# Performance work log

Hardware: AMD Instinct MI355X
Metric: run time of the kernel (lower is better)

Reference implementation:

```python
import jax, jax.numpy as jnp
import numpy as np

N_NODES = 100000
N_EDGES = 1600000
D_IN = 128
D_OUT = 128
SLOPE = 0.2


def setup_inputs() -> dict:
    key = jax.random.key(0)
    k1, k2, k3, k4 = jax.random.split(key, 4)
    x = jax.random.normal(k1, (N_NODES, D_IN), dtype=jnp.float32)
    edge_index = jax.random.randint(k2, (2, N_EDGES), 0, N_NODES, dtype=jnp.int64)
    scale = 1.0 / np.sqrt(D_IN)
    W_l = jax.random.normal(k3, (D_OUT, D_IN), dtype=jnp.float32) * scale
    b_l = jnp.zeros((D_OUT,), dtype=jnp.float32)
    W_r = jax.random.normal(k4, (D_OUT, D_IN), dtype=jnp.float32) * scale
    return {"x": x, "edge_index": edge_index, "W_l": W_l, "b_l": b_l, "W_r": W_r}


def reference(x, edge_index, W_l, b_l, W_r):
    # SAGEConv with mean aggregation: out = lin_l(mean_{j in N(i)} x_j) + lin_r(x_i)
    src = edge_index[0]  # message sources (x_j)
    dst = edge_index[1]  # aggregation targets (node i)
    n = x.shape[0]
    msg = x[src]  # [E, D_IN] gather
    summed = jax.ops.segment_sum(msg, dst, num_segments=n)  # [N, D_IN]
    cnt = jax.ops.segment_sum(jnp.ones((src.shape[0],), x.dtype), dst, num_segments=n)
    agg = summed / jnp.maximum(cnt, 1.0)[:, None]  # mean; zero-degree -> 0
    out = agg @ W_l.T + b_l + x @ W_r.T  # lin_l has bias, lin_r bias=False (PyG)
    # LeakyReLU(slope); Dropout(0.5) is identity in eval mode
    return jnp.where(out > 0, out, SLOPE * out)
```

## Files before the change

kernel.cpp:

```cpp
#include <hip/hip_runtime.h>

#define D 128
#define N_SCAN 1024
#define BSH 7
#define MAXBINS 1024

typedef float  f32x4  __attribute__((ext_vector_type(4)));
typedef short  s16x8  __attribute__((ext_vector_type(8)));
typedef unsigned short us8 __attribute__((ext_vector_type(8)));

__device__ __forceinline__ unsigned short f2bf(float f) {
    unsigned b = __float_as_uint(f);
    return (unsigned short)((b + 0x7fffu + ((b >> 16) & 1u)) >> 16);
}
__device__ __forceinline__ float bf2f(unsigned short u) {
    return __uint_as_float((unsigned)u << 16);
}

__global__ __launch_bounds__(256) void bin_hist(
    const int* __restrict__ dst, int* __restrict__ bincnt, int E, int BINS)
{
    __shared__ int h[MAXBINS];
    for (int b = threadIdx.x; b < BINS; b += 256) h[b] = 0;
    __syncthreads();
    int base = blockIdx.x * 4096;
    #pragma unroll
    for (int j = 0; j < 16; ++j) {
        int e = base + j * 256 + threadIdx.x;
        if (e < E) atomicAdd(&h[dst[e] >> BSH], 1);
    }
    __syncthreads();
    for (int b = threadIdx.x; b < BINS; b += 256)
        if (h[b]) atomicAdd(&bincnt[b], h[b]);
}

__global__ __launch_bounds__(256) void bin_scan(
    const int* __restrict__ bincnt, int* __restrict__ binptr,
    int* __restrict__ binhead, int* __restrict__ rowptr,
    int BINS, int N, int E)
{
    __shared__ int sl[256];
    const int t = threadIdx.x;
    int v[4];
    int s = 0;
    #pragma unroll
    for (int j = 0; j < 4; ++j) {
        int i = t * 4 + j;
        int c = (i < BINS) ? bincnt[i] : 0;
        v[j] = s;
        s += c;
    }
    sl[t] = s;
    __syncthreads();
    for (int off = 1; off < 256; off <<= 1) {
        int add = (t >= off) ? sl[t - off] : 0;
        __syncthreads();
        sl[t] += add;
        __syncthreads();
    }
    int excl = sl[t] - s;
    #pragma unroll
    for (int j = 0; j < 4; ++j) {
        int i = t * 4 + j;
        if (i < BINS) { binptr[i] = excl + v[j]; binhead[i] = excl + v[j]; }
    }
    if (t == 0) { binptr[BINS] = E; rowptr[N] = E; }
}

__global__ __launch_bounds__(256) void partition_edges(
    const int* __restrict__ src, const int* __restrict__ dst,
    int* __restrict__ binhead, unsigned* __restrict__ packed_g, int E, int BINS)
{
    __shared__ int h[MAXBINS];
    __shared__ int goff[MAXBINS];
    __shared__ int fill[MAXBINS];
    const int t = threadIdx.x;
    for (int b = t; b < BINS; b += 256) { h[b] = 0; fill[b] = 0; }
    __syncthreads();
    int base = blockIdx.x * 4096;
    int eb[16];
    unsigned pk[16];
    #pragma unroll
    for (int j = 0; j < 16; ++j) {
        int e = base + j * 256 + t;
        if (e < E) {
            int d = dst[e], s = src[e];
            eb[j] = d >> BSH;
            pk[j] = ((unsigned)(d & ((1 << BSH) - 1)) << 17) | (unsigned)s;
            atomicAdd(&h[eb[j]], 1);
        } else eb[j] = -1;
    }
    __syncthreads();
    for (int b = t; b < BINS; b += 256)
        if (h[b]) goff[b] = atomicAdd(&binhead[b], h[b]);
    __syncthreads();
    #pragma unroll
    for (int j = 0; j < 16; ++j) {
        if (eb[j] >= 0) {
            int p = goff[eb[j]] + atomicAdd(&fill[eb[j]], 1);
            packed_g[p] = pk[j];
        }
    }
}

__global__ __launch_bounds__(256) void bin_finalize(
    const unsigned* __restrict__ packed_g, const int* __restrict__ binptr,
    int* __restrict__ rowptr, int* __restrict__ srcs, int N)
{
    const int bin = blockIdx.x, t = threadIdx.x;
    const int beg = binptr[bin], end = binptr[bin + 1];
    const int node0 = bin << BSH;
    __shared__ int c[128];
    __shared__ int pf[128];
    __shared__ int hd[128];
    if (t < 128) c[t] = 0;
    __syncthreads();
    for (int i = beg + t; i < end; i += 256)
        atomicAdd(&c[packed_g[i] >> 17], 1);
    __syncthreads();
    if (t < 128) pf[t] = c[t];
    __syncthreads();
    for (int off = 1; off < 128; off <<= 1) {
        int v = 0;
        if (t < 128 && t >= off) v = pf[t - off];
        __syncthreads();
        if (t < 128) pf[t] += v;
        __syncthreads();
    }
    if (t < 128) {
        int node = node0 + t;
        if (node < N) {
            int r = beg + pf[t] - c[t];
            rowptr[node] = r;
            hd[t] = r;
        }
    }
    __syncthreads();
    for (int i = beg + t; i < end; i += 256) {
        unsigned p = packed_g[i];
        int dl = p >> 17;
        int s = p & 0x1FFFF;
        int pos = atomicAdd(&hd[dl], 1);
        srcs[pos] = s << 8;
    }
}

__global__ __launch_bounds__(256) void hist_kernel(
    const int* __restrict__ dst, int* __restrict__ cnt, int E)
{
    int e = blockIdx.x * 256 + threadIdx.x;
    if (e < E) atomicAdd(&cnt[dst[e]], 1);
}

__global__ __launch_bounds__(256) void scan1_kernel(
    const int* __restrict__ cnt, int* __restrict__ rowptr,
    int* __restrict__ blocksum, int N)
{
    __shared__ int sl[256];
    const int t = threadIdx.x;
    const int base = blockIdx.x * N_SCAN + t * 4;
    int v[4];
    int s = 0;
    #pragma unroll
    for (int j = 0; j < 4; ++j) {
        int i = base + j;
        int c = (i < N) ? cnt[i] : 0;
        v[j] = s;
        s += c;
    }
    sl[t] = s;
    __syncthreads();
    for (int off = 1; off < 256; off <<= 1) {
        int add = (t >= off) ? sl[t - off] : 0;
        __syncthreads();
        sl[t] += add;
        __syncthreads();
    }
    int incl = sl[t];
    int excl = incl - s;
    #pragma unroll
    for (int j = 0; j < 4; ++j) {
        int i = base + j;
        if (i < N) rowptr[i] = excl + v[j];
    }
    if (t == 255) blocksum[blockIdx.x] = incl;
}

__global__ void scan2_kernel(const int* __restrict__ blocksum,
                             int* __restrict__ blockoff, int nblk)
{
    if (threadIdx.x == 0 && blockIdx.x == 0) {
        int s = 0;
        for (int b = 0; b < nblk; ++b) { blockoff[b] = s; s += blocksum[b]; }
    }
}

__global__ __launch_bounds__(256) void scan3_kernel(
    int* __restrict__ rowptr, const int* __restrict__ blockoff,
    int* __restrict__ head, int N, int E)
{
    int i = blockIdx.x * 256 + threadIdx.x;
    if (i < N) {
        int r = rowptr[i] + blockoff[i >> 10];
        rowptr[i] = r;
        head[i] = r;
    } else if (i == N) {
        rowptr[N] = E;
    }
}

__global__ __launch_bounds__(256) void scatter_edges(
    const int* __restrict__ src, const int* __restrict__ dst,
    int* __restrict__ head, int* __restrict__ srcs, int E)
{
    int e = blockIdx.x * 256 + threadIdx.x;
    if (e < E) {
        int pos = atomicAdd(&head[dst[e]], 1);
        srcs[pos] = src[e];
    }
}

__global__ __launch_bounds__(256) void convert_bf16(
    const float* __restrict__ x, unsigned short* __restrict__ xb, long long total)
{
    long long i = ((long long)blockIdx.x * 256 + threadIdx.x) * 8;
    if (i >= total) return;
    float4 f0 = *(const float4*)(x + i);
    float4 f1 = *(const float4*)(x + i + 4);
    us8 u;
    u[0] = f2bf(f0.x); u[1] = f2bf(f0.y); u[2] = f2bf(f0.z); u[3] = f2bf(f0.w);
    u[4] = f2bf(f1.x); u[5] = f2bf(f1.y); u[6] = f2bf(f1.z); u[7] = f2bf(f1.w);
    *(us8*)(xb + i) = u;
}

__global__ __launch_bounds__(256) void aggregate_row(
    const unsigned short* __restrict__ xb, const int* __restrict__ rowptr,
    const int* __restrict__ srcs, unsigned short* __restrict__ aggb, int N)
{
    int wid  = (blockIdx.x * 256 + threadIdx.x) >> 6;
    int lane = threadIdx.x & 63;
    if (wid >= N) return;
    const int beg = rowptr[wid], end = rowptr[wid + 1];
    const char* xbase = (const char*)xb;

    float accL = 0.f, accH = 0.f;
    for (int b = beg; b < end; b += 64) {
        int idx = b + lane;
        int srcv = srcs[idx < end ? idx : end - 1];
        int cnt = end - b; if (cnt > 64) cnt = 64;
        int i = 0;
        for (; i + 8 <= cnt; i += 8) {
            unsigned u[8];
            #pragma unroll
            for (int j = 0; j < 8; ++j) {
                int so = __builtin_amdgcn_readlane(srcv, i + j);
                u[j] = *(const unsigned*)(xbase + so + lane * 4);
            }
            #pragma unroll
            for (int j = 0; j < 8; ++j) {
                accL += __uint_as_float(u[j] << 16);
                accH += __uint_as_float(u[j] & 0xffff0000u);
            }
        }
        for (; i < cnt; ++i) {
            int so = __builtin_amdgcn_readlane(srcv, i);
            unsigned u = *(const unsigned*)(xbase + so + lane * 4);
            accL += __uint_as_float(u << 16);
            accH += __uint_as_float(u & 0xffff0000u);
        }
    }
    float inv = 1.0f / fmaxf((float)(end - beg), 1.0f);
    unsigned lo = f2bf(accL * inv);
    unsigned hi = f2bf(accH * inv);
    ((unsigned*)aggb)[(size_t)wid * 64 + lane] = lo | (hi << 16);
}

__global__ __launch_bounds__(256) void aggregate_bf16(
    const unsigned short* __restrict__ xb, const int* __restrict__ rowptr,
    const int* __restrict__ srcs, unsigned short* __restrict__ aggb, int N)
{
    int wid  = (blockIdx.x * 256 + threadIdx.x) >> 6;
    int lane = threadIdx.x & 63;
    if (wid >= N) return;
    int beg = rowptr[wid], end = rowptr[wid + 1];
    const int q  = lane >> 4;
    const int sl = lane & 15;

    float acc[8] = {};
    int e = beg;
    for (; e + 8 <= end; e += 8) {
        int s0 = srcs[e + q];
        int s1 = srcs[e + 4 + q];
        us8 v0 = *(const us8*)(xb + (long long)s0 * D + sl * 8);
        us8 v1 = *(const us8*)(xb + (long long)s1 * D + sl * 8);
        #pragma unroll
        for (int j = 0; j < 8; ++j) acc[j] += bf2f(v0[j]);
        #pragma unroll
        for (int j = 0; j < 8; ++j) acc[j] += bf2f(v1[j]);
    }
    for (; e < end; e += 4) {
        int ee = e + q;
        if (ee < end) {
            int s0 = srcs[ee];
            us8 v0 = *(const us8*)(xb + (long long)s0 * D + sl * 8);
            #pragma unroll
            for (int j = 0; j < 8; ++j) acc[j] += bf2f(v0[j]);
        }
    }
    #pragma unroll
    for (int j = 0; j < 8; ++j) {
        acc[j] += __shfl_xor(acc[j], 16, 64);
        acc[j] += __shfl_xor(acc[j], 32, 64);
    }
    float inv = 1.0f / fmaxf((float)(end - beg), 1.0f);
    if (q == 0) {
        us8 u;
        #pragma unroll
        for (int j = 0; j < 8; ++j) u[j] = f2bf(acc[j] * inv);
        *(us8*)(aggb + (long long)wid * D + sl * 8) = u;
    }
}

__global__ __launch_bounds__(256) void convert_w_frag(
    const float* __restrict__ Wl, const float* __restrict__ Wr,
    unsigned short* __restrict__ wbf)
{
    int c = blockIdx.x * 256 + threadIdx.x;
    if (c >= 4096) return;
    int l  = c & 63;
    int ts = c >> 6;
    int t  = ts >> 3, s = ts & 7;
    int o  = t * 16 + (l & 15);
    int k2 = s * 32 + (l >> 4) * 8;
    const float* srcw = (k2 < 128) ? (Wl + o * D + k2) : (Wr + o * D + (k2 - 128));
    float4 f0 = *(const float4*)(srcw);
    float4 f1 = *(const float4*)(srcw + 4);
    us8 u;
    u[0] = f2bf(f0.x); u[1] = f2bf(f0.y); u[2] = f2bf(f0.z); u[3] = f2bf(f0.w);
    u[4] = f2bf(f1.x); u[5] = f2bf(f1.y); u[6] = f2bf(f1.z); u[7] = f2bf(f1.w);
    ((us8*)wbf)[c] = u;
}

__global__ __launch_bounds__(256) void mm_mfma3(
    const unsigned short* __restrict__ xb,
    const unsigned short* __restrict__ aggb,
    const unsigned short* __restrict__ wfrag,
    const float* __restrict__ bl,
    float* __restrict__ out, int N)
{
    const int tid  = threadIdx.x;
    const int lane = tid & 63;
    const int wv   = tid >> 6;
    const long long m0 = (long long)blockIdx.x * 128 + wv * 32;
    const int arow = lane & 15;
    const int kq   = lane >> 4;
    const long long r0 = m0 + arow;
    const long long r1 = m0 + 16 + arow;
    const bool v0 = (r0 < N), v1 = (r1 < N);
    const unsigned short* a0 = aggb + r0 * D + kq * 8;
    const unsigned short* x0 = xb   + r0 * D + kq * 8;
    const unsigned short* a1 = aggb + r1 * D + kq * 8;
    const unsigned short* x1 = xb   + r1 * D + kq * 8;
    const s16x8* wf = (const s16x8*)wfrag;

    f32x4 acc0[8] = {};
    f32x4 acc1[8] = {};

    #pragma unroll
    for (int s = 0; s < 8; ++s) {
        s16x8 af0 = {0, 0, 0, 0, 0, 0, 0, 0};
        s16x8 af1 = {0, 0, 0, 0, 0, 0, 0, 0};
        if (v0) af0 = *(const s16x8*)((s < 4) ? (a0 + s * 32) : (x0 + (s - 4) * 32));
        if (v1) af1 = *(const s16x8*)((s < 4) ? (a1 + s * 32) : (x1 + (s - 4) * 32));
        #pragma unroll
        for (int t = 0; t < 8; ++t) {
            s16x8 bf = wf[(t * 8 + s) * 64 + lane];
            acc0[t] = __builtin_amdgcn_mfma_f32_16x16x32_bf16(af0, bf, acc0[t], 0, 0, 0);
            acc1[t] = __builtin_amdgcn_mfma_f32_16x16x32_bf16(af1, bf, acc1[t], 0, 0, 0);
        }
    }

    const int crow = (lane >> 4) * 4;
    const int ccol = lane & 15;
    #pragma unroll
    for (int t = 0; t < 8; ++t) {
        int col = t * 16 + ccol;
        float bb = bl[col];
        #pragma unroll
        for (int r = 0; r < 4; ++r) {
            long long row0 = m0 + crow + r;
            if (row0 < N) {
                float vv = acc0[t][r] + bb;
                out[row0 * D + col] = vv > 0.f ? vv : 0.2f * vv;
            }
            long long row1 = m0 + 16 + crow + r;
            if (row1 < N) {
                float vv = acc1[t][r] + bb;
                out[row1 * D + col] = vv > 0.f ? vv : 0.2f * vv;
            }
        }
    }
}

__global__ __launch_bounds__(256) void mm_mfma(
    const unsigned short* __restrict__ xb,
    const unsigned short* __restrict__ aggb,
    const float* __restrict__ Wl, const float* __restrict__ bl,
    const float* __restrict__ Wr,
    float* __restrict__ out, int N)
{
    __shared__ char wlds[64 * 1024];
    const int tid = threadIdx.x;

    for (int c = tid; c < 4096; c += 256) {
        int byte = c * 16;
        int o  = byte >> 9;
        int k2 = (byte & 511) >> 1;
        const float* srcw = (k2 < 128) ? (Wl + o * D + k2) : (Wr + o * D + (k2 - 128));
        float4 f0 = *(const float4*)(srcw);
        float4 f1 = *(const float4*)(srcw + 4);
        us8 u;
        u[0] = f2bf(f0.x); u[1] = f2bf(f0.y); u[2] = f2bf(f0.z); u[3] = f2bf(f0.w);
        u[4] = f2bf(f1.x); u[5] = f2bf(f1.y); u[6] = f2bf(f1.z); u[7] = f2bf(f1.w);
        *(us8*)(wlds + (byte ^ ((o & 7) << 4))) = u;
    }
    __syncthreads();

    const int lane = tid & 63;
    const int wv   = tid >> 6;
    const long long m0 = (long long)blockIdx.x * 64 + wv * 16;
    const int arow = lane & 15;
    const int kq   = lane >> 4;
    const long long mrow = m0 + arow;
    const bool valid = (mrow < N);
    const unsigned short* aP = aggb + mrow * D + kq * 8;
    const unsigned short* xP = xb   + mrow * D + kq * 8;

    f32x4 acc[8] = {};

    #pragma unroll
    for (int s = 0; s < 8; ++s) {
        s16x8 afrag = {0, 0, 0, 0, 0, 0, 0, 0};
        if (valid) {
            const unsigned short* ap = (s < 4) ? (aP + s * 32) : (xP + (s - 4) * 32);
            afrag = *(const s16x8*)ap;
        }
        #pragma unroll
        for (int t = 0; t < 8; ++t) {
            int o = t * 16 + arow;
            int boff = (o << 9) + s * 64 + kq * 16;
            boff ^= (o & 7) << 4;
            s16x8 bfrag = *(const s16x8*)(wlds + boff);
            acc[t] = __builtin_amdgcn_mfma_f32_16x16x32_bf16(afrag, bfrag, acc[t], 0, 0, 0);
        }
    }

    const int crow = (lane >> 4) * 4;
    const int ccol = lane & 15;
    #pragma unroll
    for (int t = 0; t < 8; ++t) {
        int col = t * 16 + ccol;
        float bb = bl[col];
        #pragma unroll
        for (int r = 0; r < 4; ++r) {
            long long row = m0 + crow + r;
            if (row < N) {
                float v = acc[t][r] + bb;
                out[row * D + col] = v > 0.f ? v : 0.2f * v;
            }
        }
    }
}

__global__ __launch_bounds__(256) void aggregate_f32(
    const float* __restrict__ x, const int* __restrict__ rowptr,
    const int* __restrict__ srcs, float* __restrict__ out, int N)
{
    int wid  = (blockIdx.x * 256 + threadIdx.x) >> 6;
    int lane = threadIdx.x & 63;
    if (wid >= N) return;
    int beg = rowptr[wid], end = rowptr[wid + 1];
    const float2* x2 = (const float2*)x;
    float ax = 0.f, ay = 0.f;
    int e = beg;
    for (; e + 4 <= end; e += 4) {
        int s0 = srcs[e], s1 = srcs[e + 1], s2 = srcs[e + 2], s3 = srcs[e + 3];
        float2 v0 = x2[(long long)s0 * 64 + lane];
        float2 v1 = x2[(long long)s1 * 64 + lane];
        float2 v2 = x2[(long long)s2 * 64 + lane];
        float2 v3 = x2[(long long)s3 * 64 + lane];
        ax += v0.x + v1.x + v2.x + v3.x;
        ay += v0.y + v1.y + v2.y + v3.y;
    }
    for (; e < end; ++e) {
        float2 v = x2[(long long)srcs[e] * 64 + lane];
        ax += v.x; ay += v.y;
    }
    float inv = 1.0f / fmaxf((float)(end - beg), 1.0f);
    float2 o; o.x = ax * inv; o.y = ay * inv;
    ((float2*)out)[(long long)wid * 64 + lane] = o;
}

#define MT 32
#define KT 32
__global__ __launch_bounds__(256) void sage_mm_f32(
    const float* __restrict__ x, const float* __restrict__ Wl,
    const float* __restrict__ bl, const float* __restrict__ Wr,
    float* __restrict__ out, int N)
{
    __shared__ __align__(16) float a_s[KT][MT + 4];
    __shared__ __align__(16) float x_s[KT][MT + 4];
    __shared__ __align__(16) float wl_s[KT][D + 4];
    __shared__ __align__(16) float wr_s[KT][D + 4];

    const int tid = threadIdx.x;
    const int tx = tid & 31;
    const int ty = tid >> 5;
    const int node0 = blockIdx.x * MT;

    float acc[4][4] = {};

    for (int k0 = 0; k0 < D; k0 += KT) {
        __syncthreads();
        for (int i = tid; i < MT * KT; i += 256) {
            int n = i >> 5, kk = i & 31;
            int node = node0 + n;
            float av = 0.f, xv = 0.f;
            if (node < N) {
                av = out[(long long)node * D + k0 + kk];
                xv = x[(long long)node * D + k0 + kk];
            }
            a_s[kk][n] = av;
            x_s[kk][n] = xv;
        }
        for (int i = tid; i < D * KT; i += 256) {
            int o = i >> 5, kk = i & 31;
            wl_s[kk][o] = Wl[o * D + k0 + kk];
            wr_s[kk][o] = Wr[o * D + k0 + kk];
        }
        __syncthreads();
        #pragma unroll
        for (int kk = 0; kk < KT; ++kk) {
            float4 a4 = *(const float4*)&a_s[kk][ty * 4];
            float4 x4 = *(const float4*)&x_s[kk][ty * 4];
            float4 l4 = *(const float4*)&wl_s[kk][tx * 4];
            float4 r4 = *(const float4*)&wr_s[kk][tx * 4];
            float an[4] = {a4.x, a4.y, a4.z, a4.w};
            float xn[4] = {x4.x, x4.y, x4.z, x4.w};
            float lo[4] = {l4.x, l4.y, l4.z, l4.w};
            float ro[4] = {r4.x, r4.y, r4.z, r4.w};
            #pragma unroll
            for (int n = 0; n < 4; ++n)
                #pragma unroll
                for (int o = 0; o < 4; ++o)
                    acc[n][o] += an[n] * lo[o] + xn[n] * ro[o];
        }
    }

    float4 b4 = *(const float4*)&bl[tx * 4];
    float bb[4] = {b4.x, b4.y, b4.z, b4.w};
    #pragma unroll
    for (int n = 0; n < 4; ++n) {
        int node = node0 + ty * 4 + n;
        if (node < N) {
            float4 o4;
            float* po = (float*)&o4;
            #pragma unroll
            for (int o = 0; o < 4; ++o) {
                float v = acc[n][o] + bb[o];
                po[o] = v > 0.f ? v : 0.2f * v;
            }
            *(float4*)&out[(long long)node * D + tx * 4] = o4;
        }
    }
}

extern "C" void kernel_launch(void* const* d_in, const int* in_sizes, int n_in,
                              void* d_out, int out_size, void* d_ws, size_t ws_size,
                              hipStream_t stream)
{
    const float* x  = (const float*)d_in[0];
    const int*   ei = (const int*)d_in[1];
    const float* Wl = (const float*)d_in[2];
    const float* bl = (const float*)d_in[3];
    const float* Wr = (const float*)d_in[4];

    const int E = in_sizes[1] / 2;
    const int N = out_size / D;
    const int* src = ei;
    const int* dst = ei + E;
    float* out = (float*)d_out;
    const int BINS = (N + (1 << BSH) - 1) >> BSH;

    size_t off = 0;
    auto take = [&](size_t bytes) { size_t p = off; off = (off + bytes + 255) & ~(size_t)255; return p; };
    char* w = (char*)d_ws;
    int* rowptr   = (int*)(w + take((size_t)(N + 1) * 4));
    int* srcs     = (int*)(w + take((size_t)E * 4));
    int* bincnt   = (int*)(w + take((size_t)BINS * 4));
    int* binptr   = (int*)(w + take((size_t)(BINS + 1) * 4));
    int* binhead  = (int*)(w + take((size_t)BINS * 4));
    unsigned* packed = (unsigned*)(w + take((size_t)E * 4));
    unsigned short* wbf = (unsigned short*)(w + take(64 * 1024));
    unsigned short* xbf   = (unsigned short*)(w + take((size_t)N * D * 2));
    unsigned short* aggbf = (unsigned short*)(w + take((size_t)N * D * 2));
    size_t full_needed = off;

    const bool binned_ok = (BINS <= MAXBINS) && (N < (1 << 17)) && (ws_size >= full_needed);

    if (binned_ok) {
        convert_w_frag<<<16, 256, 0, stream>>>(Wl, Wr, wbf);

        hipMemsetAsync(bincnt, 0, (size_t)BINS * 4, stream);
        int pb = (E + 4095) / 4096;
        bin_hist<<<pb, 256, 0, stream>>>(dst, bincnt, E, BINS);
        bin_scan<<<1, 256, 0, stream>>>(bincnt, binptr, binhead, rowptr, BINS, N, E);
        partition_edges<<<pb, 256, 0, stream>>>(src, dst, binhead, packed, E, BINS);
        bin_finalize<<<BINS, 256, 0, stream>>>(packed, binptr, rowptr, srcs, N);

        long long total = (long long)N * D;
        int cb = (int)((total / 8 + 255) / 256);
        convert_bf16<<<cb, 256, 0, stream>>>(x, xbf, total);
        int ab = (N * 64 + 255) / 256;
        aggregate_row<<<ab, 256, 0, stream>>>(xbf, rowptr, srcs, aggbf, N);
        int mb = (N + 127) / 128;
        mm_mfma3<<<mb, 256, 0, stream>>>(xbf, aggbf, wbf, bl, out, N);
        return;
    }

    off = 0;
    int* cnt    = (int*)(w + take((size_t)N * 4));
    rowptr      = (int*)(w + take((size_t)(N + 1) * 4));
    int* head   = (int*)(w + take((size_t)N * 4));
    int* blocksum = (int*)(w + take(4096));
    int* blockoff = (int*)(w + take(4096));
    srcs        = (int*)(w + take((size_t)E * 4));
    size_t base_needed = off;
    xbf   = (unsigned short*)(w + take((size_t)N * D * 2));
    aggbf = (unsigned short*)(w + take((size_t)N * D * 2));
    size_t bf16_needed = off;

    hipMemsetAsync(cnt, 0, (size_t)N * 4, stream);
    const int eb = (E + 255) / 256;
    hist_kernel<<<eb, 256, 0, stream>>>(dst, cnt, E);
    const int nblk = (N + N_SCAN - 1) / N_SCAN;
    scan1_kernel<<<nblk, 256, 0, stream>>>(cnt, rowptr, blocksum, N);
    scan2_kernel<<<1, 64, 0, stream>>>(blocksum, blockoff, nblk);
    scan3_kernel<<<(N + 1 + 255) / 256, 256, 0, stream>>>(rowptr, blockoff, head, N, E);
    scatter_edges<<<eb, 256, 0, stream>>>(src, dst, head, srcs, E);

    if (ws_size >= bf16_needed) {
        long long total = (long long)N * D;
        int cb = (int)((total / 8 + 255) / 256);
        convert_bf16<<<cb, 256, 0, stream>>>(x, xbf, total);
        int ab = (N * 64 + 255) / 256;
        aggregate_bf16<<<ab, 256, 0, stream>>>(xbf, rowptr, srcs, aggbf, N);
        int mb = (N + 63) / 64;
        mm_mfma<<<mb, 256, 0, stream>>>(xbf, aggbf, Wl, bl, Wr, out, N);
    } else {
        (void)base_needed;
        int ab = (N * 64 + 255) / 256;
        aggregate_f32<<<ab, 256, 0, stream>>>(x, rowptr, srcs, out, N);
        sage_mm_f32<<<(N + MT - 1) / MT, 256, 0, stream>>>(x, Wl, bl, Wr, out, N);
    }
}
```

Before: 181.2 us.

## Fuse neighbor aggregation with MFMA linear layer via LDS tile

Replaces the separate aggregate_row and mm_mfma3 kernels with a single kernel. Each block aggregates 16 nodes (four per wave) into a bf16 tile in shared memory, then runs the 16x128 GEMM with each wave handling two output column tiles. This removes the global write and re-read of the N x D bf16 aggregate buffer and one kernel launch. In exchange, MFMA work per block is small, weight fragments are re-read by many more blocks, and aggregation and matmul can no longer overlap across nodes.

```diff
diff --git a/kernel.cpp b/kernel.cpp
--- a/kernel.cpp
+++ b/kernel.cpp
@@ -231,94 +231,6 @@
     u[0] = f2bf(f0.x); u[1] = f2bf(f0.y); u[2] = f2bf(f0.z); u[3] = f2bf(f0.w);
     u[4] = f2bf(f1.x); u[5] = f2bf(f1.y); u[6] = f2bf(f1.z); u[7] = f2bf(f1.w);
     *(us8*)(xb + i) = u;
-}
-
-__global__ __launch_bounds__(256) void aggregate_row(
-    const unsigned short* __restrict__ xb, const int* __restrict__ rowptr,
-    const int* __restrict__ srcs, unsigned short* __restrict__ aggb, int N)
-{
-    int wid  = (blockIdx.x * 256 + threadIdx.x) >> 6;
-    int lane = threadIdx.x & 63;
-    if (wid >= N) return;
-    const int beg = rowptr[wid], end = rowptr[wid + 1];
-    const char* xbase = (const char*)xb;
-
-    float accL = 0.f, accH = 0.f;
-    for (int b = beg; b < end; b += 64) {
-        int idx = b + lane;
-        int srcv = srcs[idx < end ? idx : end - 1];
-        int cnt = end - b; if (cnt > 64) cnt = 64;
-        int i = 0;
-        for (; i + 8 <= cnt; i += 8) {
-            unsigned u[8];
-            #pragma unroll
-            for (int j = 0; j < 8; ++j) {
-                int so = __builtin_amdgcn_readlane(srcv, i + j);
-                u[j] = *(const unsigned*)(xbase + so + lane * 4);
-            }
-            #pragma unroll
-            for (int j = 0; j < 8; ++j) {
-                accL += __uint_as_float(u[j] << 16);
-                accH += __uint_as_float(u[j] & 0xffff0000u);
-            }
-        }
-        for (; i < cnt; ++i) {
-            int so = __builtin_amdgcn_readlane(srcv, i);
-            unsigned u = *(const unsigned*)(xbase + so + lane * 4);
-            accL += __uint_as_float(u << 16);
-            accH += __uint_as_float(u & 0xffff0000u);
-        }
-    }
-    float inv = 1.0f / fmaxf((float)(end - beg), 1.0f);
-    unsigned lo = f2bf(accL * inv);
-    unsigned hi = f2bf(accH * inv);
-    ((unsigned*)aggb)[(size_t)wid * 64 + lane] = lo | (hi << 16);
-}
-
-__global__ __launch_bounds__(256) void aggregate_bf16(
-    const unsigned short* __restrict__ xb, const int* __restrict__ rowptr,
-    const int* __restrict__ srcs, unsigned short* __restrict__ aggb, int N)
-{
-    int wid  = (blockIdx.x * 256 + threadIdx.x) >> 6;
-    int lane = threadIdx.x & 63;
-    if (wid >= N) return;
-    int beg = rowptr[wid], end = rowptr[wid + 1];
-    const int q  = lane >> 4;
-    const int sl = lane & 15;
-
-    float acc[8] = {};
-    int e = beg;
-    for (; e + 8 <= end; e += 8) {
-        int s0 = srcs[e + q];
-        int s1 = srcs[e + 4 + q];
-        us8 v0 = *(const us8*)(xb + (long long)s0 * D + sl * 8);
-        us8 v1 = *(const us8*)(xb + (long long)s1 * D + sl * 8);
-        #pragma unroll
-        for (int j = 0; j < 8; ++j) acc[j] += bf2f(v0[j]);
-        #pragma unroll
-        for (int j = 0; j < 8; ++j) acc[j] += bf2f(v1[j]);
-    }
-    for (; e < end; e += 4) {
-        int ee = e + q;
-        if (ee < end) {
-            int s0 = srcs[ee];
-            us8 v0 = *(const us8*)(xb + (long long)s0 * D + sl * 8);
-            #pragma unroll
-            for (int j = 0; j < 8; ++j) acc[j] += bf2f(v0[j]);
-        }
-    }
-    #pragma unroll
-    for (int j = 0; j < 8; ++j) {
-        acc[j] += __shfl_xor(acc[j], 16, 64);
-        acc[j] += __shfl_xor(acc[j], 32, 64);
-    }
-    float inv = 1.0f / fmaxf((float)(end - beg), 1.0f);
-    if (q == 0) {
-        us8 u;
-        #pragma unroll
-        for (int j = 0; j < 8; ++j) u[j] = f2bf(acc[j] * inv);
-        *(us8*)(aggb + (long long)wid * D + sl * 8) = u;
-    }
 }
 
 __global__ __launch_bounds__(256) void convert_w_frag(
@@ -341,64 +253,146 @@
     ((us8*)wbf)[c] = u;
 }
 
-__global__ __launch_bounds__(256) void mm_mfma3(
-    const unsigned short* __restrict__ xb,
-    const unsigned short* __restrict__ aggb,
-    const unsigned short* __restrict__ wfrag,
-    const float* __restrict__ bl,
-    float* __restrict__ out, int N)
-{
+__global__ __launch_bounds__(256) void fused_agg_mm(
+    const unsigned short* __restrict__ xb, const int* __restrict__ rowptr,
+    const int* __restrict__ srcs, const unsigned short* __restrict__ wfrag,
+    const float* __restrict__ bl, float* __restrict__ out, int N)
+{
+    __shared__ unsigned short agg_lds[16][136];
     const int tid  = threadIdx.x;
     const int lane = tid & 63;
     const int wv   = tid >> 6;
-    const long long m0 = (long long)blockIdx.x * 128 + wv * 32;
+    const int m0   = blockIdx.x * 16;
     const int arow = lane & 15;
     const int kq   = lane >> 4;
-    const long long r0 = m0 + arow;
-    const long long r1 = m0 + 16 + arow;
-    const bool v0 = (r0 < N), v1 = (r1 < N);
-    const unsigned short* a0 = aggb + r0 * D + kq * 8;
-    const unsigned short* x0 = xb   + r0 * D + kq * 8;
-    const unsigned short* a1 = aggb + r1 * D + kq * 8;
-    const unsigned short* x1 = xb   + r1 * D + kq * 8;
+
+    const int xrow = m0 + arow;
+    const bool vr = (xrow < N);
+    s16x8 xf[4];
+    #pragma unroll
+    for (int s = 0; s < 4; ++s) {
+        s16x8 z = {0, 0, 0, 0, 0, 0, 0, 0};
+        xf[s] = z;
+        if (vr) xf[s] = *(const s16x8*)(xb + (size_t)xrow * D + s * 32 + kq * 8);
+    }
+
+    const char* xbase = (const char*)xb;
+    #pragma unroll
+    for (int j = 0; j < 4; ++j) {
+        const int nd = wv * 4 + j;
+        const int node = m0 + nd;
+        float accL = 0.f, accH = 0.f;
+        if (node < N) {
+            const int beg = rowptr[node], end = rowptr[node + 1];
+            for (int b = beg; b < end; b += 64) {
+                int idx = b + lane;
+                int srcv = srcs[idx < end ? idx : end - 1];
+                int cnt = end - b; if (cnt > 64) cnt = 64;
+                int i = 0;
+                for (; i + 8 <= cnt; i += 8) {
+                    unsigned u[8];
+                    #pragma unroll
+                    for (int k = 0; k < 8; ++k) {
+                        int so = __builtin_amdgcn_readlane(srcv, i + k);
+                        u[k] = *(const unsigned*)(xbase + so + lane * 4);
+                    }
+                    #pragma unroll
+                    for (int k = 0; k < 8; ++k) {
+                        accL += __uint_as_float(u[k] << 16);
+                        accH += __uint_as_float(u[k] & 0xffff0000u);
+                    }
+                }
+                for (; i < cnt; ++i) {
+                    int so = __builtin_amdgcn_readlane(srcv, i);
+                    unsigned u = *(const unsigned*)(xbase + so + lane * 4);
+                    accL += __uint_as_float(u << 16);
+                    accH += __uint_as_float(u & 0xffff0000u);
+                }
+            }
+            float inv = 1.0f / fmaxf((float)(end - beg), 1.0f);
+            accL *= inv; accH *= inv;
+        }
+        unsigned lo = f2bf(accL);
+        unsigned hi = f2bf(accH);
+        *(unsigned*)&agg_lds[nd][lane * 2] = lo | (hi << 16);
+    }
+    __syncthreads();
+
     const s16x8* wf = (const s16x8*)wfrag;
-
-    f32x4 acc0[8] = {};
-    f32x4 acc1[8] = {};
-
+    f32x4 acc[2] = {};
     #pragma unroll
     for (int s = 0; s < 8; ++s) {
-        s16x8 af0 = {0, 0, 0, 0, 0, 0, 0, 0};
-        s16x8 af1 = {0, 0, 0, 0, 0, 0, 0, 0};
-        if (v0) af0 = *(const s16x8*)((s < 4) ? (a0 + s * 32) : (x0 + (s - 4) * 32));
-        if (v1) af1 = *(const s16x8*)((s < 4) ? (a1 + s * 32) : (x1 + (s - 4) * 32));
-        #pragma unroll
-        for (int t = 0; t < 8; ++t) {
+        s16x8 af;
+        if (s < 4) af = *(const s16x8*)&agg_lds[arow][s * 32 + kq * 8];
+        else       af = xf[s - 4];
+        #pragma unroll
+        for (int ti = 0; ti < 2; ++ti) {
+            int t = wv * 2 + ti;
             s16x8 bf = wf[(t * 8 + s) * 64 + lane];
-            acc0[t] = __builtin_amdgcn_mfma_f32_16x16x32_bf16(af0, bf, acc0[t], 0, 0, 0);
-            acc1[t] = __builtin_amdgcn_mfma_f32_16x16x32_bf16(af1, bf, acc1[t], 0, 0, 0);
+            acc[ti] = __builtin_amdgcn_mfma_f32_16x16x32_bf16(af, bf, acc[ti], 0, 0, 0);
         }
     }
 
     const int crow = (lane >> 4) * 4;
     const int ccol = lane & 15;
     #pragma unroll
-    for (int t = 0; t < 8; ++t) {
-        int col = t * 16 + ccol;
+    for (int ti = 0; ti < 2; ++ti) {
+        int col = (wv * 2 + ti) * 16 + ccol;
         float bb = bl[col];
         #pragma unroll
         for (int r = 0; r < 4; ++r) {
-            long long row0 = m0 + crow + r;
-            if (row0 < N) {
-                float vv = acc0[t][r] + bb;
-                out[row0 * D + col] = vv > 0.f ? vv : 0.2f * vv;
+            int row = m0 + crow + r;
+            if (row < N) {
+                float vv = acc[ti][r] + bb;
+                out[(size_t)row * D + col] = vv > 0.f ? vv : 0.2f * vv;
             }
-            long long row1 = m0 + 16 + crow + r;
-            if (row1 < N) {
-                float vv = acc1[t][r] + bb;
-                out[row1 * D + col] = vv > 0.f ? vv : 0.2f * vv;
-            }
-        }
+        }
+    }
+}
+
+__global__ __launch_bounds__(256) void aggregate_bf16(
+    const unsigned short* __restrict__ xb, const int* __restrict__ rowptr,
+    const int* __restrict__ srcs, unsigned short* __restrict__ aggb, int N)
+{
+    int wid  = (blockIdx.x * 256 + threadIdx.x) >> 6;
+    int lane = threadIdx.x & 63;
+    if (wid >= N) return;
+    int beg = rowptr[wid], end = rowptr[wid + 1];
+    const int q  = lane >> 4;
+    const int sl = lane & 15;
+
+    float acc[8] = {};
+    int e = beg;
+    for (; e + 8 <= end; e += 8) {
+        int s0 = srcs[e + q];
+        int s1 = srcs[e + 4 + q];
+        us8 v0 = *(const us8*)(xb + (long long)s0 * D + sl * 8);
+        us8 v1 = *(const us8*)(xb + (long long)s1 * D + sl * 8);
+        #pragma unroll
+        for (int j = 0; j < 8; ++j) acc[j] += bf2f(v0[j]);
+        #pragma unroll
+        for (int j = 0; j < 8; ++j) acc[j] += bf2f(v1[j]);
+    }
+    for (; e < end; e += 4) {
+        int ee = e + q;
+        if (ee < end) {
+            int s0 = srcs[ee];
+            us8 v0 = *(const us8*)(xb + (long long)s0 * D + sl * 8);
+            #pragma unroll
+            for (int j = 0; j < 8; ++j) acc[j] += bf2f(v0[j]);
+        }
+    }
+    #pragma unroll
+    for (int j = 0; j < 8; ++j) {
+        acc[j] += __shfl_xor(acc[j], 16, 64);
+        acc[j] += __shfl_xor(acc[j], 32, 64);
+    }
+    float inv = 1.0f / fmaxf((float)(end - beg), 1.0f);
+    if (q == 0) {
+        us8 u;
+        #pragma unroll
+        for (int j = 0; j < 8; ++j) u[j] = f2bf(acc[j] * inv);
+        *(us8*)(aggb + (long long)wid * D + sl * 8) = u;
     }
 }
 
@@ -602,13 +596,12 @@
     int* binhead  = (int*)(w + take((size_t)BINS * 4));
     unsigned* packed = (unsigned*)(w + take((size_t)E * 4));
     unsigned short* wbf = (unsigned short*)(w + take(64 * 1024));
-    unsigned short* xbf   = (unsigned short*)(w + take((size_t)N * D * 2));
-    unsigned short* aggbf = (unsigned short*)(w + take((size_t)N * D * 2));
-    size_t full_needed = off;
-
-    const bool binned_ok = (BINS <= MAXBINS) && (N < (1 << 17)) && (ws_size >= full_needed);
-
-    if (binned_ok) {
+    unsigned short* xbf = (unsigned short*)(w + take((size_t)N * D * 2));
+    size_t fused_needed = off;
+
+    const bool fused_ok = (BINS <= MAXBINS) && (N < (1 << 17)) && (ws_size >= fused_needed);
+
+    if (fused_ok) {
         convert_w_frag<<<16, 256, 0, stream>>>(Wl, Wr, wbf);
 
         hipMemsetAsync(bincnt, 0, (size_t)BINS * 4, stream);
@@ -621,10 +614,8 @@
         long long total = (long long)N * D;
         int cb = (int)((total / 8 + 255) / 256);
         convert_bf16<<<cb, 256, 0, stream>>>(x, xbf, total);
-        int ab = (N * 64 + 255) / 256;
-        aggregate_row<<<ab, 256, 0, stream>>>(xbf, rowptr, srcs, aggbf, N);
-        int mb = (N + 127) / 128;
-        mm_mfma3<<<mb, 256, 0, stream>>>(xbf, aggbf, wbf, bl, out, N);
+        int fb = (N + 15) / 16;
+        fused_agg_mm<<<fb, 256, 0, stream>>>(xbf, rowptr, srcs, wbf, bl, out, N);
         return;
     }
 
@@ -637,7 +628,7 @@
     srcs        = (int*)(w + take((size_t)E * 4));
     size_t base_needed = off;
     xbf   = (unsigned short*)(w + take((size_t)N * D * 2));
-    aggbf = (unsigned short*)(w + take((size_t)N * D * 2));
+    unsigned short* aggbf = (unsigned short*)(w + take((size_t)N * D * 2));
     size_t bf16_needed = off;
 
     hipMemsetAsync(cnt, 0, (size_t)N * 4, stream);
```

Result: faster. 162.1 us (-10.6%).
